# Performance work log

Hardware: AMD Instinct MI355X
Metric: run time of the kernel (lower is better)

## Reference

```python
import jax, jax.numpy as jnp
import numpy as np

B, G, D_EMB = 4096, 20000, 512
H_LOW, N_HIDDEN = 512, 1024
TOPK, T, FILM_W = 64, 0.1, 1.0
LN_EPS = 1e-5


def _layer_norm(x, gamma, beta):
    mu = jnp.mean(x, axis=-1, keepdims=True)
    var = jnp.mean(jnp.square(x - mu), axis=-1, keepdims=True)
    return (x - mu) * jax.lax.rsqrt(var + LN_EPS) * gamma + beta


def _l2norm(x, eps=1e-12):
    n = jnp.sqrt(jnp.sum(jnp.square(x), axis=-1, keepdims=True))
    return x / jnp.maximum(n, eps)


def setup_inputs() -> dict:
    key = jax.random.key(0)
    ks = jax.random.split(key, 8)
    s = 0.02
    return {
        "x": jax.random.normal(ks[0], (B, G), jnp.float32),
        "g": jax.random.normal(ks[1], (G, D_EMB), jnp.float32),
        "W_enc": jax.random.normal(ks[2], (H_LOW, G), jnp.float32) * s,
        "b_enc": jnp.zeros((H_LOW,), jnp.float32),
        "ln1_g": jnp.ones((H_LOW,), jnp.float32),
        "ln1_b": jnp.zeros((H_LOW,), jnp.float32),
        "W_ga": jax.random.normal(ks[3], (H_LOW, D_EMB), jnp.float32) * s,
        "W_gamma": jax.random.normal(ks[4], (H_LOW, H_LOW), jnp.float32) * s,
        "b_gamma": jnp.zeros((H_LOW,), jnp.float32),
        "W_beta": jax.random.normal(ks[5], (H_LOW, H_LOW), jnp.float32) * s,
        "b_beta": jnp.zeros((H_LOW,), jnp.float32),
        "W_exp": jax.random.normal(ks[6], (N_HIDDEN, H_LOW), jnp.float32) * s,
        "b_exp": jnp.zeros((N_HIDDEN,), jnp.float32),
        "ln2_g": jnp.ones((N_HIDDEN,), jnp.float32),
        "ln2_b": jnp.zeros((N_HIDDEN,), jnp.float32),
    }


def reference(x, g, W_enc, b_enc, ln1_g, ln1_b, W_ga, W_gamma, b_gamma,
              W_beta, b_beta, W_exp, b_exp, ln2_g, ln2_b):
    # x_encoder: Linear -> LayerNorm -> GELU (dropout = eval no-op)
    h = jnp.dot(x, W_enc.T) + b_enc                    # [B, H_LOW]
    h = jax.nn.gelu(_layer_norm(h, ln1_g, ln1_b), approximate=False)
    # gene adapter + cosine scores
    e = _l2norm(jnp.dot(g, W_ga.T))                    # [G, H_LOW]
    h_x = _l2norm(h)                                   # [B, H_LOW]
    scores = jnp.dot(h_x, e.T) / T                     # [B, G]
    # top-k mask + masked softmax attention
    _, idx = jax.lax.top_k(scores, TOPK)               # [B, TOPK]
    mask = jnp.zeros_like(scores).at[jnp.arange(B)[:, None], idx].set(1.0)
    attn = jax.nn.softmax(jnp.where(mask == 0, -1e9, scores), axis=-1)
    ctx = jnp.dot(attn, e)                             # [B, H_LOW]
    # FiLM (identity-centered)
    gamma = (jnp.dot(ctx, W_gamma.T) + b_gamma) * FILM_W
    beta = (jnp.dot(ctx, W_beta.T) + b_beta) * FILM_W
    h_cell = (1.0 + gamma) * h_x + beta
    # x_expand: Linear -> LayerNorm -> GELU
    h2 = jnp.dot(h_cell, W_exp.T) + b_exp              # [B, N_HIDDEN]
    return jax.nn.gelu(_layer_norm(h2, ln2_g, ln2_b), approximate=False)
```

## Files before the change

kernel.cpp:

```cpp
#include <hip/hip_runtime.h>
#include <hip/hip_fp16.h>
#include <math.h>
#include <type_traits>

#define DEVI __device__ __forceinline__

typedef __attribute__((ext_vector_type(8))) short bf16x8;
typedef __attribute__((ext_vector_type(4))) float f32x4;
typedef __attribute__((ext_vector_type(4))) unsigned int u32x4;
typedef unsigned short ushort_t;

DEVI unsigned int pack_bf16(float a, float b) {
  unsigned int ua = __float_as_uint(a), ub = __float_as_uint(b);
  ua = (ua + 0x7FFFu + ((ua >> 16) & 1u)) >> 16;
  ub = (ub + 0x7FFFu + ((ub >> 16) & 1u)) >> 16;
  return ua | (ub << 16);
}

DEVI bf16x8 cvt_bf16x8(f32x4 lo, f32x4 hi) {
  unsigned int r0, r1, r2, r3;
  asm("v_cvt_pk_bf16_f32 %0, %1, %2" : "=v"(r0) : "v"(lo[0]), "v"(lo[1]));
  asm("v_cvt_pk_bf16_f32 %0, %1, %2" : "=v"(r1) : "v"(lo[2]), "v"(lo[3]));
  asm("v_cvt_pk_bf16_f32 %0, %1, %2" : "=v"(r2) : "v"(hi[0]), "v"(hi[1]));
  asm("v_cvt_pk_bf16_f32 %0, %1, %2" : "=v"(r3) : "v"(hi[2]), "v"(hi[3]));
  union { u32x4 u; bf16x8 v; } x;
  x.u = u32x4{r0, r1, r2, r3};
  return x.v;
}

template<int SPLITZ, bool TAIL>
__global__ __launch_bounds__(512, 1) void bgemmA32(
    const float* __restrict__ A, const ushort_t* __restrict__ B,
    float* __restrict__ C, int M, int N, int K, int nbn, int nbm)
{
  __shared__ __align__(16) char L[131072];
  const int tid = threadIdx.x, lane = tid & 63, wv = tid >> 6;

  const int nwg = gridDim.x;
  const int hw = blockIdx.x;
  const int q = nwg >> 3, r = nwg & 7;
  const int xcd = hw & 7, pos = hw >> 3;
  const int lid = (xcd < r ? xcd * (q + 1) : r * (q + 1) + (xcd - r) * q) + pos;
  const int bn = lid % nbn;
  const int t2 = lid / nbn;
  const int bm = t2 % nbm;
  const int z  = t2 / nbm;

  const int ksteps = K >> 6;
  const int szk = (ksteps + SPLITZ - 1) / SPLITZ;
  const int kbBeg = z * szk;
  const int kbEnd = min(ksteps, kbBeg + szk);

  const int wm = wv >> 2, wn = wv & 3;
  const int lrow = lane & 15, kg = lane >> 4;

  f32x4 acc[4][4];
#pragma unroll
  for (int i = 0; i < 4; ++i)
#pragma unroll
    for (int j = 0; j < 4; ++j) acc[i][j] = f32x4{0.f, 0.f, 0.f, 0.f};

  const int alr = lane >> 3, ag32 = (lane & 7) >> 1;
  const float* aS[2];
#pragma unroll
  for (int j = 0; j < 2; ++j) {
    const int lr = (wv * 2 + j) * 8 + alr;
    const int swz = (lr ^ (lr >> 2)) & 3;
    const int colf = ((ag32 ^ swz) << 3) + (lane & 1) * 4;
    aS[j] = A + (size_t)min(bm * 128 + lr, M - 1) * (size_t)K + colf;
  }
  const int blr = lane >> 2, bgq = lane & 3;
  const ushort_t* bS[2];
#pragma unroll
  for (int j = 0; j < 2; ++j) {
    const int lr = (wv * 2 + j) * 16 + blr;
    const int swz = (lr ^ (lr >> 2)) & 3;
    aS[j] = aS[j];
    bS[j] = B + (size_t)min(bn * 256 + lr, N - 1) * (size_t)K + ((bgq ^ swz) << 3);
  }

  int offA[4], offB[4];
#pragma unroll
  for (int i = 0; i < 4; ++i) {
    const int ra = wm * 64 + i * 16 + lrow;
    offA[i] = ra * 128 + ((kg ^ ((ra ^ (ra >> 2)) & 3)) << 5);
  }
#pragma unroll
  for (int j = 0; j < 4; ++j) {
    const int rb = wn * 64 + j * 16 + lrow;
    offB[j] = rb * 64 + ((kg ^ ((rb ^ (rb >> 2)) & 3)) << 4);
  }

#define GA_STGA(h, k0v) do {                                                  \
    _Pragma("unroll")                                                         \
    for (int j_ = 0; j_ < 2; ++j_)                                            \
      __builtin_amdgcn_global_load_lds(                                       \
          (const __attribute__((address_space(1))) void*)(aS[j_] + (k0v) + (h) * 32), \
          (__attribute__((address_space(3))) void*)                           \
              (L + (s ^ 1) * 32768 + (h) * 16384 + (wv * 2 + j_) * 1024),     \
          16, 0, 0);                                                          \
  } while (0)
#define GA_STGB(h, k0v) do {                                                  \
    _Pragma("unroll")                                                         \
    for (int j_ = 0; j_ < 2; ++j_)                                            \
      __builtin_amdgcn_global_load_lds(                                       \
          (const __attribute__((address_space(1))) void*)(bS[j_] + (k0v) + (h) * 32), \
          (__attribute__((address_space(3))) void*)                           \
              (L + 65536 + (s ^ 1) * 32768 + (h) * 16384 + (wv * 2 + j_) * 1024), \
          16, 0, 0);                                                          \
  } while (0)
#define GA_RDB(h) do {                                                        \
    _Pragma("unroll")                                                         \
    for (int j_ = 0; j_ < 4; ++j_)                                            \
      bfv[j_] = *(const bf16x8*)(L + 65536 + s * 32768 + (h) * 16384 + offB[j_]); \
  } while (0)
#define GA_RDA(h, rg) do {                                                    \
    _Pragma("unroll")                                                         \
    for (int i_ = 0; i_ < 2; ++i_) {                                          \
      const char* pa_ = L + s * 32768 + (h) * 16384 + offA[(rg) * 2 + i_];    \
      af[i_] = cvt_bf16x8(*(const f32x4*)pa_, *(const f32x4*)(pa_ + 16));     \
    }                                                                         \
  } while (0)
#define GA_MM(rg) do {                                                        \
    _Pragma("unroll")                                                         \
    for (int i_ = 0; i_ < 2; ++i_)                                            \
      _Pragma("unroll")                                                       \
      for (int j_ = 0; j_ < 4; ++j_)                                          \
        acc[(rg) * 2 + i_][j_] = __builtin_amdgcn_mfma_f32_16x16x32_bf16(     \
            af[i_], bfv[j_], acc[(rg) * 2 + i_][j_], 0, 0, 0);                \
  } while (0)
#define GA_BAR asm volatile("s_barrier" ::: "memory")

  {
    int s = 1;
    const int k0 = kbBeg << 6;
    GA_STGA(0, k0); GA_STGB(0, k0); GA_STGA(1, k0); GA_STGB(1, k0);
  }
  asm volatile("s_waitcnt vmcnt(4)" ::: "memory");
  GA_BAR;

  int s = 0;
  for (int t = kbBeg; t < kbEnd; ++t) {
    const bool more = (t + 1 < kbEnd);
    const int k0n = (t + 1) << 6;
    bf16x8 af[2], bfv[4];
    GA_RDB(0); GA_RDA(0, 0);
    if (more) GA_STGA(0, k0n);
    GA_BAR;
    __builtin_amdgcn_s_setprio(1); GA_MM(0); __builtin_amdgcn_s_setprio(0);
    GA_BAR;
    GA_RDA(0, 1);
    if (more) GA_STGB(0, k0n);
    GA_BAR;
    __builtin_amdgcn_s_setprio(1); GA_MM(1); __builtin_amdgcn_s_setprio(0);
    if (more) asm volatile("s_waitcnt vmcnt(4)" ::: "memory");
    else      asm volatile("s_waitcnt vmcnt(0)" ::: "memory");
    GA_BAR;
    GA_RDB(1); GA_RDA(1, 0);
    if (more) GA_STGA(1, k0n);
    GA_BAR;
    __builtin_amdgcn_s_setprio(1); GA_MM(0); __builtin_amdgcn_s_setprio(0);
    GA_BAR;
    GA_RDA(1, 1);
    if (more) GA_STGB(1, k0n);
    GA_BAR;
    __builtin_amdgcn_s_setprio(1); GA_MM(1); __builtin_amdgcn_s_setprio(0);
    if (more) asm volatile("s_waitcnt vmcnt(4)" ::: "memory");
    GA_BAR;
    s ^= 1;
  }

  if (TAIL && z == SPLITZ - 1 && (K & 63)) {
    const int k0t = ksteps << 6;
    bf16x8 af[2], bfv[4];
#pragma unroll
    for (int j = 0; j < 2; ++j) {
      const float4 av = *(const float4*)(aS[j] + k0t);
      *(float4*)(L + s * 32768 + (wv * 2 + j) * 1024 + lane * 16) = av;
      const u32x4 bv = *(const u32x4*)(bS[j] + k0t);
      *(u32x4*)(L + 65536 + s * 32768 + (wv * 2 + j) * 1024 + lane * 16) = bv;
    }
    __syncthreads();
    GA_RDB(0);
    GA_RDA(0, 0); GA_MM(0);
    GA_RDA(0, 1); GA_MM(1);
  }
#undef GA_STGA
#undef GA_STGB
#undef GA_RDB
#undef GA_RDA
#undef GA_MM
#undef GA_BAR

  const size_t zoff = (SPLITZ > 1) ? (size_t)z * (size_t)M * (size_t)N : 0;
#pragma unroll
  for (int i = 0; i < 4; ++i) {
#pragma unroll
    for (int j = 0; j < 4; ++j) {
      const int col = bn * 256 + wn * 64 + j * 16 + lrow;
      if (col >= N) continue;
      const int row0 = bm * 128 + wm * 64 + i * 16 + kg * 4;
#pragma unroll
      for (int rr = 0; rr < 4; ++rr) {
        const int gr = row0 + rr;
        if (gr < M) C[zoff + (size_t)gr * (size_t)N + col] = acc[i][j][rr];
      }
    }
  }
}

template<int SPLITZ, typename OutT>
__global__ __launch_bounds__(512, 1) void bgemm256(
    const ushort_t* __restrict__ A, const ushort_t* __restrict__ B,
    OutT* __restrict__ C, int M, int N, int K, int nbn, int nbm)
{
  __shared__ __align__(16) char L[131072];
  const int tid = threadIdx.x, lane = tid & 63, wv = tid >> 6;

  const int nwg = gridDim.x;
  const int hw = blockIdx.x;
  const int q = nwg >> 3, r = nwg & 7;
  const int xcd = hw & 7, pos = hw >> 3;
  const int lid = (xcd < r ? xcd * (q + 1) : r * (q + 1) + (xcd - r) * q) + pos;
  const int bn = lid % nbn;
  const int t2 = lid / nbn;
  const int bm = t2 % nbm;
  const int z  = t2 / nbm;

  const int ksteps = K >> 6;
  int kbBeg = 0, kbEnd = ksteps;
  if (SPLITZ > 1) {
    const int sz = (ksteps + SPLITZ - 1) / SPLITZ;
    kbBeg = z * sz;
    kbEnd = min(ksteps, kbBeg + sz);
  }

  const int wm = wv >> 2, wn = wv & 3;
  const int lrow = lane & 15, kg = lane >> 4;

  f32x4 acc[8][4];
#pragma unroll
  for (int i = 0; i < 8; ++i)
#pragma unroll
    for (int j = 0; j < 4; ++j) acc[i][j] = f32x4{0.f, 0.f, 0.f, 0.f};

  const int sr = lane >> 2, sq = lane & 3;
  const ushort_t* aS[2];
  const ushort_t* bS[2];
#pragma unroll
  for (int j = 0; j < 2; ++j) {
    const int lr = (wv * 2 + j) * 16 + sr;
    const int swz = (lr ^ (lr >> 2)) & 3;
    aS[j] = A + (size_t)min(bm * 256 + lr, M - 1) * (size_t)K + ((sq ^ swz) << 3);
    bS[j] = B + (size_t)min(bn * 256 + lr, N - 1) * (size_t)K + ((sq ^ swz) << 3);
  }

  int offA[8], offB[4];
#pragma unroll
  for (int i = 0; i < 8; ++i) {
    const int ra = wm * 128 + i * 16 + lrow;
    offA[i] = ra * 64 + (((kg ^ ((ra ^ (ra >> 2)) & 3))) << 4);
  }
#pragma unroll
  for (int j = 0; j < 4; ++j) {
    const int rb = wn * 64 + j * 16 + lrow;
    offB[j] = rb * 64 + (((kg ^ ((rb ^ (rb >> 2)) & 3))) << 4);
  }

#define G256_STG(isB, h, k0v) do {                                            \
    _Pragma("unroll")                                                         \
    for (int j_ = 0; j_ < 2; ++j_)                                            \
      __builtin_amdgcn_global_load_lds(                                       \
          (const __attribute__((address_space(1))) void*)                     \
              (((isB) ? bS : aS)[j_] + (k0v) + (h) * 32),                     \
          (__attribute__((address_space(3))) void*)                           \
              (L + (isB) * 65536 + (s ^ 1) * 32768 + (h) * 16384 +            \
               (wv * 2 + j_) * 1024), 16, 0, 0);                              \
  } while (0)
#define G256_RDA(h, rg) do {                                                  \
    _Pragma("unroll")                                                         \
    for (int i_ = 0; i_ < 4; ++i_)                                            \
      af[i_] = *(const bf16x8*)(L + s * 32768 + (h) * 16384 +                 \
                                offA[(rg) * 4 + i_]);                         \
  } while (0)
#define G256_RDB(h) do {                                                      \
    _Pragma("unroll")                                                         \
    for (int j_ = 0; j_ < 4; ++j_)                                            \
      bfv[j_] = *(const bf16x8*)(L + 65536 + s * 32768 + (h) * 16384 +        \
                                 offB[j_]);                                   \
  } while (0)
#define G256_MM(rg) do {                                                      \
    _Pragma("unroll")                                                         \
    for (int i_ = 0; i_ < 4; ++i_)                                            \
      _Pragma("unroll")                                                       \
      for (int j_ = 0; j_ < 4; ++j_)                                          \
        acc[(rg) * 4 + i_][j_] = __builtin_amdgcn_mfma_f32_16x16x32_bf16(     \
            af[i_], bfv[j_], acc[(rg) * 4 + i_][j_], 0, 0, 0);                \
  } while (0)
#define G256_BAR asm volatile("s_barrier" ::: "memory")

  {
    int s = 1;
    const int k0 = kbBeg << 6;
    G256_STG(0, 0, k0);
    G256_STG(1, 0, k0);
    G256_STG(0, 1, k0);
    G256_STG(1, 1, k0);
  }
  asm volatile("s_waitcnt vmcnt(4)" ::: "memory");
  G256_BAR;

  int s = 0;
  for (int t = kbBeg; t < kbEnd; ++t) {
    const bool more = (t + 1 < kbEnd);
    const int k0n = (t + 1) << 6;
    bf16x8 af[4], bfv[4];
    G256_RDB(0);
    G256_RDA(0, 0);
    if (more) G256_STG(0, 0, k0n);
    G256_BAR;
    __builtin_amdgcn_s_setprio(1); G256_MM(0); __builtin_amdgcn_s_setprio(0);
    G256_BAR;
    G256_RDA(0, 1);
    if (more) G256_STG(1, 0, k0n);
    G256_BAR;
    __builtin_amdgcn_s_setprio(1); G256_MM(1); __builtin_amdgcn_s_setprio(0);
    if (more) asm volatile("s_waitcnt vmcnt(4)" ::: "memory");
    else      asm volatile("s_waitcnt vmcnt(0)" ::: "memory");
    G256_BAR;
    G256_RDB(1);
    G256_RDA(1, 0);
    if (more) G256_STG(0, 1, k0n);
    G256_BAR;
    __builtin_amdgcn_s_setprio(1); G256_MM(0); __builtin_amdgcn_s_setprio(0);
    G256_BAR;
    G256_RDA(1, 1);
    if (more) G256_STG(1, 1, k0n);
    G256_BAR;
    __builtin_amdgcn_s_setprio(1); G256_MM(1); __builtin_amdgcn_s_setprio(0);
    if (more) asm volatile("s_waitcnt vmcnt(4)" ::: "memory");
    G256_BAR;
    s ^= 1;
  }
#undef G256_STG
#undef G256_RDA
#undef G256_RDB
#undef G256_MM
#undef G256_BAR

  const size_t zoff = (SPLITZ > 1) ? (size_t)z * (size_t)M * (size_t)N : 0;
#pragma unroll
  for (int i = 0; i < 8; ++i) {
#pragma unroll
    for (int j = 0; j < 4; ++j) {
      const int col = bn * 256 + wn * 64 + j * 16 + lrow;
      if (col >= N) continue;
      const int row0 = bm * 256 + wm * 128 + i * 16 + kg * 4;
#pragma unroll
      for (int rr = 0; rr < 4; ++rr) {
        const int gr = row0 + rr;
        if (gr < M) {
          const float v = acc[i][j][rr];
          if constexpr (std::is_same<OutT, __half>::value)
            C[zoff + (size_t)gr * (size_t)N + col] = __float2half(v);
          else
            C[zoff + (size_t)gr * (size_t)N + col] = v;
        }
      }
    }
  }
}

template<typename AT, int SPLITZ, bool DUALB, bool BIAS, typename OutT>
__global__ __launch_bounds__(512, sizeof(AT) == 2 ? 3 : 2) void bgemm(
    const AT* __restrict__ A, const ushort_t* __restrict__ B0,
    const ushort_t* __restrict__ B1, const float* __restrict__ bias0,
    const float* __restrict__ bias1, OutT* __restrict__ C,
    int M, int N, int K, int nbn, int nbm)
{
  constexpr bool AB16 = (sizeof(AT) == 2);
  __shared__ __align__(16) char AsB[AB16 ? 16384 : 32768];
  __shared__ __align__(16) char BsB[32768];
  const int tid = threadIdx.x, lane = tid & 63, wv = tid >> 6;

  const int nwg = gridDim.x;
  const int hw = blockIdx.x;
  const int q = nwg >> 3, r = nwg & 7;
  const int xcd = hw & 7, pos = hw >> 3;
  const int lid = (xcd < r ? xcd * (q + 1) : r * (q + 1) + (xcd - r) * q) + pos;
  const int bn = lid % nbn;
  const int t2 = lid / nbn;
  const int bm = t2 % nbm;
  const int z  = t2 / nbm;

  const ushort_t* B  = (DUALB && z == 1) ? B1 : B0;
  const float* bias  = (DUALB && z == 1) ? bias1 : bias0;

  const int ksteps = (K + 63) >> 6;
  int kbBeg = 0, kbEnd = ksteps;
  if (SPLITZ > 1) {
    const int sz = (ksteps + SPLITZ - 1) / SPLITZ;
    kbBeg = z * sz;
    kbEnd = min(ksteps, kbBeg + sz);
  }

  const int wr = (wv >> 2) * 64;
  const int wc = (wv & 3) * 64;
  const int lrow = lane & 15, kg = lane >> 4;

  f32x4 acc[4][4];
#pragma unroll
  for (int i = 0; i < 4; ++i)
#pragma unroll
    for (int j = 0; j < 4; ++j) acc[i][j] = f32x4{0.f, 0.f, 0.f, 0.f};

  const AT* aSrc[4];
  if constexpr (AB16) {
    const int r0 = lane >> 3;
    const int ce = ((lane & 7) ^ r0) << 3;
#pragma unroll
    for (int j = 0; j < 2; ++j) {
      const int row = wv * 16 + j * 8 + r0;
      aSrc[j] = A + (size_t)min(bm * 128 + row, M - 1) * (size_t)K + ce;
    }
  } else {
    const int r0 = lane >> 4;
#pragma unroll
    for (int j = 0; j < 4; ++j) {
      const int row = wv * 16 + j * 4 + r0;
      const int ca = ((lane & 15) << 2) ^ ((row & 7) << 3);
      aSrc[j] = A + (size_t)min(bm * 128 + row, M - 1) * (size_t)K + ca;
    }
  }
  const int rB0 = lane >> 3;
  const int colB = ((lane & 7) ^ rB0) << 3;
  const ushort_t* bSrc[4];
#pragma unroll
  for (int j = 0; j < 4; ++j) {
    const int row = wv * 32 + j * 8 + rB0;
    bSrc[j] = B + (size_t)min(bn * 256 + row, N - 1) * (size_t)K + colB;
  }

  for (int kb = kbBeg; kb < kbEnd; ++kb) {
    const int k0 = kb << 6;
    if constexpr (AB16) {
#pragma unroll
      for (int j = 0; j < 2; ++j)
        __builtin_amdgcn_global_load_lds(
            (const __attribute__((address_space(1))) void*)(aSrc[j] + k0),
            (__attribute__((address_space(3))) void*)(AsB + (wv * 2 + j) * 1024),
            16, 0, 0);
    } else {
#pragma unroll
      for (int j = 0; j < 4; ++j)
        __builtin_amdgcn_global_load_lds(
            (const __attribute__((address_space(1))) void*)(aSrc[j] + k0),
            (__attribute__((address_space(3))) void*)(AsB + (wv * 4 + j) * 1024),
            16, 0, 0);
    }
#pragma unroll
    for (int j = 0; j < 4; ++j)
      __builtin_amdgcn_global_load_lds(
          (const __attribute__((address_space(1))) void*)(bSrc[j] + k0),
          (__attribute__((address_space(3))) void*)(BsB + (wv * 4 + j) * 1024),
          16, 0, 0);
    __syncthreads();
#pragma unroll
    for (int kk = 0; kk < 2; ++kk) {
      bf16x8 af[4], bfr[4];
#pragma unroll
      for (int i = 0; i < 4; ++i) {
        const int ra = wr + i * 16 + lrow;
        if constexpr (AB16) {
          af[i] = *(const bf16x8*)(AsB + ra * 128 + ((((kk << 2) + kg) ^ (ra & 7)) << 4));
        } else {
          const char* pa = AsB + ra * 256 + ((kk * 128 + (kg << 5)) ^ ((ra & 7) << 5));
          af[i] = cvt_bf16x8(*(const f32x4*)pa, *(const f32x4*)(pa + 16));
        }
        const int rb = wc + i * 16 + lrow;
        bfr[i] = *(const bf16x8*)(BsB + rb * 128 + ((((kk << 2) + kg) ^ (rb & 7)) << 4));
      }
#pragma unroll
      for (int i = 0; i < 4; ++i)
#pragma unroll
        for (int j = 0; j < 4; ++j)
          acc[i][j] = __builtin_amdgcn_mfma_f32_16x16x32_bf16(af[i], bfr[j], acc[i][j], 0, 0, 0);
    }
    __syncthreads();
  }

  const size_t zoff = (SPLITZ > 1 || DUALB) ? (size_t)z * (size_t)M * (size_t)N : 0;
#pragma unroll
  for (int i = 0; i < 4; ++i) {
#pragma unroll
    for (int j = 0; j < 4; ++j) {
      const int col = bn * 256 + wc + j * 16 + lrow;
      if (col >= N) continue;
      const int row0 = bm * 128 + wr + i * 16 + kg * 4;
      float bv = 0.f;
      if (BIAS) bv = bias[col];
#pragma unroll
      for (int rr = 0; rr < 4; ++rr) {
        const int gr = row0 + rr;
        if (gr < M) {
          const float v = acc[i][j][rr] + bv;
          if constexpr (std::is_same<OutT, __half>::value)
            C[zoff + (size_t)gr * (size_t)N + col] = __float2half(v);
          else
            C[zoff + (size_t)gr * (size_t)N + col] = v;
        }
      }
    }
  }
}

__global__ __launch_bounds__(256) void f2b(
    const float4* __restrict__ in, u32x4* __restrict__ out, int n8)
{
  const int i = blockIdx.x * 256 + threadIdx.x;
  if (i < n8) {
    const float4 a = in[2 * i], b = in[2 * i + 1];
    u32x4 o = { pack_bf16(a.x, a.y), pack_bf16(a.z, a.w),
                pack_bf16(b.x, b.y), pack_bf16(b.z, b.w) };
    out[i] = o;
  }
}

__global__ __launch_bounds__(256) void gee_fuse_ln1(
    const float* __restrict__ P, const float* __restrict__ b_enc,
    const float* __restrict__ g1, const float* __restrict__ b1,
    float* __restrict__ hx, unsigned int* __restrict__ hxb)
{
  const int row = blockIdx.x, tid = threadIdx.x;
  __shared__ float red[16];
  const size_t MN = (size_t)4096 * 512;
  const size_t o2 = (size_t)row * 256 + tid;
  float2 v = ((const float2*)b_enc)[tid];
#pragma unroll
  for (int qq = 0; qq < 4; ++qq) {
    const float2 p = ((const float2*)P)[qq * (MN / 2) + o2];
    v.x += p.x; v.y += p.y;
  }
  float a = v.x + v.y;
  float b = v.x * v.x + v.y * v.y;
#pragma unroll
  for (int o = 32; o > 0; o >>= 1) { a += __shfl_xor(a, o); b += __shfl_xor(b, o); }
  const int lane = tid & 63, wvi = tid >> 6;
  if (lane == 0) { red[wvi] = a; red[8 + wvi] = b; }
  __syncthreads();
  const float mu  = (red[0] + red[1] + red[2] + red[3]) * (1.f / 512.f);
  const float ex2 = (red[8] + red[9] + red[10] + red[11]) * (1.f / 512.f);
  const float inv = rsqrtf(ex2 - mu * mu + 1e-5f);
  const float2 gg = ((const float2*)g1)[tid];
  const float2 bb = ((const float2*)b1)[tid];
  const float y0 = (v.x - mu) * inv * gg.x + bb.x;
  const float y1 = (v.y - mu) * inv * gg.y + bb.y;
  const float t0 = 0.5f * y0 * (1.f + erff(y0 * 0.70710678118654752f));
  const float t1 = 0.5f * y1 * (1.f + erff(y1 * 0.70710678118654752f));
  float ss = t0 * t0 + t1 * t1;
  __syncthreads();
#pragma unroll
  for (int o = 32; o > 0; o >>= 1) ss += __shfl_xor(ss, o);
  if (lane == 0) red[wvi] = ss;
  __syncthreads();
  const float sc = 1.f / fmaxf(sqrtf(red[0] + red[1] + red[2] + red[3]), 1e-12f);
  const float h0 = t0 * sc, h1 = t1 * sc;
  ((float2*)hx)[o2] = make_float2(h0, h1);
  hxb[o2] = pack_bf16(h0, h1);
}

__global__ __launch_bounds__(256) void gee_l2rows(
    const __half2* __restrict__ ein, unsigned int* __restrict__ eb)
{
  const int row = blockIdx.x, tid = threadIdx.x;
  __shared__ float red[4];
  const __half2 h = ein[(size_t)row * 256 + tid];
  const float vx = __half2float(h.x), vy = __half2float(h.y);
  float ss = vx * vx + vy * vy;
#pragma unroll
  for (int o = 32; o > 0; o >>= 1) ss += __shfl_xor(ss, o);
  if ((tid & 63) == 0) red[tid >> 6] = ss;
  __syncthreads();
  const float sc = 1.f / fmaxf(sqrtf(red[0] + red[1] + red[2] + red[3]), 1e-12f);
  eb[(size_t)row * 256 + tid] = pack_bf16(vx * sc, vy * sc);
}

__global__ __launch_bounds__(256) void gee_topk_ctx(
    const __half* __restrict__ scores, const unsigned int* __restrict__ eb,
    unsigned int* __restrict__ ctxb)
{
  constexpr int G = 20000, GP = G / 2, CAP = 2048, TCAP = 160;
  const int row = blockIdx.x, tid = threadIdx.x;
  const int lane = tid & 63, wv = tid >> 6;
  __shared__ int hist[4][256];
  __shared__ int cnt_ge[256];
  __shared__ int wtop[4];
  __shared__ unsigned int comp[CAP];
  __shared__ int whist[4][16];
  __shared__ int sel[64];
  __shared__ float swt[64];
  __shared__ int tie[TCAP];
  __shared__ int s_thr, s_above, s_cand, s_cnt, s_n1, s_n2;

  const unsigned int* srow32 =
      (const unsigned int*)((const ushort_t*)scores + (size_t)row * G);
  const ushort_t* srow16 = (const ushort_t*)srow32;

#pragma unroll
  for (int b = 0; b < 4; ++b) hist[b][tid] = 0;
  if (tid == 0) { s_cnt = 0; s_n1 = 0; s_n2 = 0; }
  __syncthreads();

  for (int j0 = 0; j0 < GP; j0 += 256) {
    const int j = j0 + tid;
    if (j < GP) {
      const unsigned int p = srow32[j];
      const unsigned int f = (((p >> 15) & 0x10001u) * 0x7FFFu) + 0x80008000u;
      const unsigned int k2 = p ^ f;
      atomicAdd(&hist[wv][(k2 >> 8) & 0xFFu], 1);
      atomicAdd(&hist[wv][k2 >> 24], 1);
    }
  }
  __syncthreads();
  cnt_ge[tid] = hist[0][tid] + hist[1][tid] + hist[2][tid] + hist[3][tid];
  __syncthreads();
  for (int off = 1; off < 256; off <<= 1) {
    const int add = (tid + off < 256) ? cnt_ge[tid + off] : 0;
    __syncthreads();
    cnt_ge[tid] += add;
    __syncthreads();
  }
  {
    const unsigned long long m = __ballot(cnt_ge[tid] >= 64);
    if (lane == 0) wtop[wv] = m ? (wv * 64 + 63 - __clzll(m)) : -1;
  }
  __syncthreads();
  if (tid == 0) {
    const int thrB = max(max(wtop[0], wtop[1]), max(wtop[2], wtop[3]));
    s_cand  = cnt_ge[thrB];
    s_above = (thrB == 255) ? 0 : cnt_ge[thrB + 1];
    s_thr   = thrB << 8;
  }
  __syncthreads();

  const bool useComp = (s_cand <= CAP);
  const unsigned int thrB = ((unsigned int)s_thr) >> 8;

  if (useComp) {
    for (int j0 = 0; j0 < GP; j0 += 256) {
      const int j = j0 + tid;
      if (j < GP) {
        const unsigned int p = srow32[j];
        const unsigned int f = (((p >> 15) & 0x10001u) * 0x7FFFu) + 0x80008000u;
        const unsigned int k2 = p ^ f;
        const unsigned int lo = k2 & 0xFFFFu, hi = k2 >> 16;
        if ((lo >> 8) >= thrB) {
          const int pos = atomicAdd(&s_cnt, 1);
          comp[pos] = (lo << 16) | (unsigned)(2 * j);
        }
        if ((hi >> 8) >= thrB) {
          const int pos = atomicAdd(&s_cnt, 1);
          comp[pos] = (hi << 16) | (unsigned)(2 * j + 1);
        }
      }
    }
  }
  __syncthreads();
  const int Nloop = useComp ? s_cnt : G;

  for (int pass = 2; pass < 4; ++pass) {
    const int shift = 12 - 4 * pass;
    const unsigned int thr = (unsigned int)s_thr;
    const unsigned int pfx = thr >> (shift + 4);
    int c[16];
#pragma unroll
    for (int b = 0; b < 16; ++b) c[b] = 0;
    for (int j0 = 0; j0 < Nloop; j0 += 256) {
      const int j = j0 + tid;
      const bool ok = j < Nloop;
      unsigned int key;
      if (useComp) {
        key = ok ? (comp[j] >> 16) : 0u;
      } else {
        const unsigned int raw = ok ? (unsigned int)srow16[j] : 0u;
        key = (raw & 0x8000u) ? (0xFFFFu & ~raw) : (raw | 0x8000u);
      }
      const unsigned int nb = (ok && (key >> (shift + 4)) == pfx) ? ((key >> shift) & 15u) : 0xFFu;
#pragma unroll
      for (int b = 0; b < 16; ++b) c[b] += __popcll(__ballot(nb == (unsigned)b));
    }
    if (lane == 0) {
#pragma unroll
      for (int b = 0; b < 16; ++b) whist[wv][b] = c[b];
    }
    __syncthreads();
    if (tid == 0) {
      int run = s_above;
      for (int vv = 15; vv >= 0; --vv) {
        const int c4 = whist[0][vv] + whist[1][vv] + whist[2][vv] + whist[3][vv];
        if (run + c4 >= 64) { s_thr |= vv << shift; break; }
        run += c4;
      }
      s_above = run;
    }
    __syncthreads();
  }

  const unsigned int kthr = (unsigned int)s_thr;
  for (int j0 = 0; j0 < Nloop; j0 += 256) {
    const int j = j0 + tid;
    if (j < Nloop) {
      unsigned int key, idx;
      if (useComp) {
        const unsigned int u = comp[j];
        key = u >> 16; idx = u & 0xFFFFu;
      } else {
        const unsigned int raw = (unsigned int)srow16[j];
        key = (raw & 0x8000u) ? (0xFFFFu & ~raw) : (raw | 0x8000u);
        idx = (unsigned)j;
      }
      if (key > kthr) {
        const int pos = atomicAdd(&s_n1, 1);
        sel[pos] = (int)idx;
      } else if (key == kthr) {
        const int pos = atomicAdd(&s_n2, 1);
        if (pos < TCAP) tie[pos] = (int)idx;
      }
    }
  }
  __syncthreads();
  if (tid == 0) {
    const int n1 = s_n1;
    const int n2 = min(s_n2, TCAP);
    const int need = 64 - n1;
    for (int rr = 0; rr < need; ++rr) {
      int best = 1 << 30, bj = 0;
      for (int j = 0; j < n2; ++j)
        if (tie[j] < best) { best = tie[j]; bj = j; }
      sel[n1 + rr] = best;
      tie[bj] = 1 << 30;
    }
  }
  __syncthreads();
  if (tid < 64) {
    const int idx = sel[tid];
    const float sv = __half2float(scores[(size_t)row * G + idx]) * 10.0f;
    float m = sv;
#pragma unroll
    for (int o = 32; o > 0; o >>= 1) m = fmaxf(m, __shfl_xor(m, o));
    const float w = __expf(sv - m);
    float d = w;
#pragma unroll
    for (int o = 32; o > 0; o >>= 1) d += __shfl_xor(d, o);
    swt[tid] = w / d;
  }
  __syncthreads();
  float a0 = 0.f, a1 = 0.f;
#pragma unroll 4
  for (int k = 0; k < 64; ++k) {
    const unsigned int pk = eb[(size_t)sel[k] * 256 + tid];
    const float wk = swt[k];
    a0 += wk * __uint_as_float(pk << 16);
    a1 += wk * __uint_as_float(pk & 0xFFFF0000u);
  }
  ctxb[(size_t)row * 256 + tid] = pack_bf16(a0, a1);
}

__global__ __launch_bounds__(256) void gee_film(
    const float2* __restrict__ gm, const float2* __restrict__ bt,
    const float2* __restrict__ hx, unsigned int* __restrict__ hcb, int n2)
{
  const int i = blockIdx.x * 256 + threadIdx.x;
  if (i < n2) {
    const float2 g = gm[i], b = bt[i], h = hx[i];
    hcb[i] = pack_bf16((1.f + g.x) * h.x + b.x, (1.f + g.y) * h.y + b.y);
  }
}

__global__ __launch_bounds__(256) void gee_ln2(
    const float* __restrict__ h2, const float* __restrict__ g2,
    const float* __restrict__ b2, float* __restrict__ out)
{
  const int row = blockIdx.x, tid = threadIdx.x;
  __shared__ float red[16];
  float v[4];
  float a = 0.f, b = 0.f;
#pragma unroll
  for (int e = 0; e < 4; ++e) {
    v[e] = h2[(size_t)row * 1024 + tid + e * 256];
    a += v[e]; b += v[e] * v[e];
  }
#pragma unroll
  for (int o = 32; o > 0; o >>= 1) { a += __shfl_xor(a, o); b += __shfl_xor(b, o); }
  const int lane = tid & 63, wvi = tid >> 6;
  if (lane == 0) { red[wvi] = a; red[8 + wvi] = b; }
  __syncthreads();
  const float mu  = (red[0] + red[1] + red[2] + red[3]) * (1.f / 1024.f);
  const float ex2 = (red[8] + red[9] + red[10] + red[11]) * (1.f / 1024.f);
  const float inv = rsqrtf(ex2 - mu * mu + 1e-5f);
#pragma unroll
  for (int e = 0; e < 4; ++e) {
    const int c = tid + e * 256;
    const float y = (v[e] - mu) * inv * g2[c] + b2[c];
    out[(size_t)row * 1024 + c] = 0.5f * y * (1.f + erff(y * 0.70710678118654752f));
  }
}

extern "C" void kernel_launch(void* const* d_in, const int* in_sizes, int n_in,
                              void* d_out, int out_size, void* d_ws, size_t ws_size,
                              hipStream_t stream)
{
  const float* x       = (const float*)d_in[0];
  const float* g       = (const float*)d_in[1];
  const float* W_enc   = (const float*)d_in[2];
  const float* b_enc   = (const float*)d_in[3];
  const float* ln1_g   = (const float*)d_in[4];
  const float* ln1_b   = (const float*)d_in[5];
  const float* W_ga    = (const float*)d_in[6];
  const float* W_gamma = (const float*)d_in[7];
  const float* b_gamma = (const float*)d_in[8];
  const float* W_beta  = (const float*)d_in[9];
  const float* b_beta  = (const float*)d_in[10];
  const float* W_exp   = (const float*)d_in[11];
  const float* b_exp   = (const float*)d_in[12];
  const float* ln2_g   = (const float*)d_in[13];
  const float* ln2_b   = (const float*)d_in[14];
  float* out = (float*)d_out;

  char* ws = (char*)d_ws;
  constexpr size_t OFF_SCORES = 0;
  constexpr size_t OFF_GA     = 0;
  constexpr size_t OFF_BE     = 8388608;
  constexpr size_t OFF_H2     = 16777216;
  constexpr size_t OFF_PART   = 163840000;
  constexpr size_t OFF_WENCB  = 197394432;
  constexpr size_t OFF_E      = 197394432;
  constexpr size_t OFF_EB     = 217874432;
  constexpr size_t OFF_HX     = 238354432;
  constexpr size_t OFF_HXB    = 246743040;
  constexpr size_t OFF_CTXB   = 250937344;
  constexpr size_t OFF_HCB    = 255131648;
  constexpr size_t OFF_WGAB   = 259325952;
  constexpr size_t OFF_WGMB   = 259850240;
  constexpr size_t OFF_WBTB   = 260374528;
  constexpr size_t OFF_WEXB   = 260898816;

  __half*       scores = (__half*)(ws + OFF_SCORES);
  float*        ga     = (float*)(ws + OFF_GA);
  float*        be     = (float*)(ws + OFF_BE);
  float*        h2     = (float*)(ws + OFF_H2);
  float*        part   = (float*)(ws + OFF_PART);
  ushort_t*     wencb  = (ushort_t*)(ws + OFF_WENCB);
  __half*       e      = (__half*)(ws + OFF_E);
  unsigned int* eb     = (unsigned int*)(ws + OFF_EB);
  float*        hx     = (float*)(ws + OFF_HX);
  unsigned int* hxb    = (unsigned int*)(ws + OFF_HXB);
  unsigned int* ctxb   = (unsigned int*)(ws + OFF_CTXB);
  unsigned int* hcb    = (unsigned int*)(ws + OFF_HCB);
  ushort_t*     wgab   = (ushort_t*)(ws + OFF_WGAB);
  ushort_t*     wgmb   = (ushort_t*)(ws + OFF_WGMB);
  ushort_t*     wbtb   = (ushort_t*)(ws + OFF_WBTB);
  ushort_t*     wexb   = (ushort_t*)(ws + OFF_WEXB);

  f2b<<<5000, 256, 0, stream>>>((const float4*)W_enc,   (u32x4*)wencb, 1280000);
  f2b<<<128,  256, 0, stream>>>((const float4*)W_ga,    (u32x4*)wgab,  32768);
  f2b<<<128,  256, 0, stream>>>((const float4*)W_gamma, (u32x4*)wgmb,  32768);
  f2b<<<128,  256, 0, stream>>>((const float4*)W_beta,  (u32x4*)wbtb,  32768);
  f2b<<<256,  256, 0, stream>>>((const float4*)W_exp,   (u32x4*)wexb,  65536);

  bgemmA32<4, true><<<256, 512, 0, stream>>>(
      x, wencb, part, 4096, 512, 20000, 2, 32);
  gee_fuse_ln1<<<4096, 256, 0, stream>>>(part, b_enc, ln1_g, ln1_b, hx, hxb);
  bgemm<float, 1, false, false, __half><<<314, 512, 0, stream>>>(
      g, wgab, nullptr, nullptr, nullptr, e, 20000, 512, 512, 2, 157);
  gee_l2rows<<<20000, 256, 0, stream>>>((const __half2*)e, eb);
  bgemm256<1, __half><<<1264, 512, 0, stream>>>(
      (const ushort_t*)hxb, (const ushort_t*)eb, scores, 4096, 20000, 512, 79, 16);
  gee_topk_ctx<<<4096, 256, 0, stream>>>(scores, eb, ctxb);
  bgemm<ushort_t, 1, true, true, float><<<128, 512, 0, stream>>>(
      (const ushort_t*)ctxb, wgmb, wbtb, b_gamma, b_beta, ga, 4096, 512, 512, 2, 32);
  gee_film<<<4096, 256, 0, stream>>>((const float2*)ga, (const float2*)be,
                                     (const float2*)hx, hcb, 1048576);
  bgemm<ushort_t, 1, false, true, float><<<128, 512, 0, stream>>>(
      (const ushort_t*)hcb, wexb, nullptr, b_exp, nullptr, h2, 4096, 1024, 512, 4, 32);
  gee_ln2<<<4096, 256, 0, stream>>>(h2, ln2_g, ln2_b, out);
}
```

Baseline: 503.9 us.

## Fuse FiLM into dual gamma/beta GEMM and speculatively collect top-k candidates

A new bgemm_film kernel computes the gamma and beta projections together, sharing the A tile, and applies the FiLM combine in its epilogue, writing bf16 h_cell directly. This removes the separate gee_film kernel and the round trip of the fp32 gamma/beta buffers through memory. The top-k kernel now reads scores in 128-bit vectors and, during the histogram pass, speculatively gathers candidates whose high byte exceeds a fixed threshold (0xAD), so the second scan can be skipped when the real threshold lands above it. The fused GEMM uses only 64 workgroups and needs more LDS and registers, so occupancy and parallelism drop, and the speculative atomics add shared-memory contention.

```diff
diff --git a/kernel.cpp b/kernel.cpp
--- a/kernel.cpp
+++ b/kernel.cpp
@@ -15,6 +15,11 @@
   ua = (ua + 0x7FFFu + ((ua >> 16) & 1u)) >> 16;
   ub = (ub + 0x7FFFu + ((ub >> 16) & 1u)) >> 16;
   return ua | (ub << 16);
+}
+
+DEVI ushort_t rnd_bf16(float a) {
+  unsigned int ua = __float_as_uint(a);
+  return (ushort_t)((ua + 0x7FFFu + ((ua >> 16) & 1u)) >> 16);
 }
 
 DEVI bf16x8 cvt_bf16x8(f32x4 lo, f32x4 hi) {
@@ -75,7 +80,6 @@
   for (int j = 0; j < 2; ++j) {
     const int lr = (wv * 2 + j) * 16 + blr;
     const int swz = (lr ^ (lr >> 2)) & 3;
-    aS[j] = aS[j];
     bS[j] = B + (size_t)min(bn * 256 + lr, N - 1) * (size_t)K + ((bgq ^ swz) << 3);
   }
 
@@ -371,11 +375,10 @@
   }
 }
 
-template<typename AT, int SPLITZ, bool DUALB, bool BIAS, typename OutT>
+template<typename AT, int SPLITZ, bool BIAS, typename OutT>
 __global__ __launch_bounds__(512, sizeof(AT) == 2 ? 3 : 2) void bgemm(
     const AT* __restrict__ A, const ushort_t* __restrict__ B0,
-    const ushort_t* __restrict__ B1, const float* __restrict__ bias0,
-    const float* __restrict__ bias1, OutT* __restrict__ C,
+    const float* __restrict__ bias0, OutT* __restrict__ C,
     int M, int N, int K, int nbn, int nbm)
 {
   constexpr bool AB16 = (sizeof(AT) == 2);
@@ -393,8 +396,8 @@
   const int bm = t2 % nbm;
   const int z  = t2 / nbm;
 
-  const ushort_t* B  = (DUALB && z == 1) ? B1 : B0;
-  const float* bias  = (DUALB && z == 1) ? bias1 : bias0;
+  const ushort_t* B  = B0;
+  const float* bias  = bias0;
 
   const int ksteps = (K + 63) >> 6;
   int kbBeg = 0, kbEnd = ksteps;
@@ -489,7 +492,7 @@
     __syncthreads();
   }
 
-  const size_t zoff = (SPLITZ > 1 || DUALB) ? (size_t)z * (size_t)M * (size_t)N : 0;
+  const size_t zoff = (SPLITZ > 1) ? (size_t)z * (size_t)M * (size_t)N : 0;
 #pragma unroll
   for (int i = 0; i < 4; ++i) {
 #pragma unroll
@@ -509,6 +512,117 @@
           else
             C[zoff + (size_t)gr * (size_t)N + col] = v;
         }
+      }
+    }
+  }
+}
+
+__global__ __launch_bounds__(512, 2) void bgemm_film(
+    const ushort_t* __restrict__ A, const ushort_t* __restrict__ BG,
+    const ushort_t* __restrict__ BB, const float* __restrict__ bg,
+    const float* __restrict__ bb, const float* __restrict__ hx,
+    ushort_t* __restrict__ hcb)
+{
+  constexpr int M = 4096, N = 512, K = 512;
+  __shared__ __align__(16) char AsB[16384];
+  __shared__ __align__(16) char BsB[65536];
+  const int tid = threadIdx.x, lane = tid & 63, wv = tid >> 6;
+
+  const int nwg = gridDim.x;
+  const int hw = blockIdx.x;
+  const int q = nwg >> 3, r = nwg & 7;
+  const int xcd = hw & 7, pos = hw >> 3;
+  const int lid = (xcd < r ? xcd * (q + 1) : r * (q + 1) + (xcd - r) * q) + pos;
+  const int bn = lid % 2;
+  const int bm = lid / 2;
+
+  const int wr = (wv >> 2) * 64;
+  const int wc = (wv & 3) * 64;
+  const int lrow = lane & 15, kg = lane >> 4;
+
+  f32x4 accG[4][4], accB[4][4];
+#pragma unroll
+  for (int i = 0; i < 4; ++i)
+#pragma unroll
+    for (int j = 0; j < 4; ++j) {
+      accG[i][j] = f32x4{0.f, 0.f, 0.f, 0.f};
+      accB[i][j] = f32x4{0.f, 0.f, 0.f, 0.f};
+    }
+
+  const int r0 = lane >> 3;
+  const int ce = ((lane & 7) ^ r0) << 3;
+  const ushort_t* aSrc[2];
+#pragma unroll
+  for (int j = 0; j < 2; ++j) {
+    const int row = wv * 16 + j * 8 + r0;
+    aSrc[j] = A + (size_t)(bm * 128 + row) * (size_t)K + ce;
+  }
+  const ushort_t* gSrc[4];
+  const ushort_t* bSrc[4];
+#pragma unroll
+  for (int j = 0; j < 4; ++j) {
+    const int row = wv * 32 + j * 8 + r0;
+    gSrc[j] = BG + (size_t)(bn * 256 + row) * (size_t)K + ce;
+    bSrc[j] = BB + (size_t)(bn * 256 + row) * (size_t)K + ce;
+  }
+
+  for (int kb = 0; kb < K / 64; ++kb) {
+    const int k0 = kb << 6;
+#pragma unroll
+    for (int j = 0; j < 2; ++j)
+      __builtin_amdgcn_global_load_lds(
+          (const __attribute__((address_space(1))) void*)(aSrc[j] + k0),
+          (__attribute__((address_space(3))) void*)(AsB + (wv * 2 + j) * 1024),
+          16, 0, 0);
+#pragma unroll
+    for (int j = 0; j < 4; ++j) {
+      __builtin_amdgcn_global_load_lds(
+          (const __attribute__((address_space(1))) void*)(gSrc[j] + k0),
+          (__attribute__((address_space(3))) void*)(BsB + (wv * 4 + j) * 1024),
+          16, 0, 0);
+      __builtin_amdgcn_global_load_lds(
+          (const __attribute__((address_space(1))) void*)(bSrc[j] + k0),
+          (__attribute__((address_space(3))) void*)(BsB + 32768 + (wv * 4 + j) * 1024),
+          16, 0, 0);
+    }
+    __syncthreads();
+#pragma unroll
+    for (int kk = 0; kk < 2; ++kk) {
+      bf16x8 af[4], bfG[4], bfB[4];
+#pragma unroll
+      for (int i = 0; i < 4; ++i) {
+        const int ra = wr + i * 16 + lrow;
+        af[i] = *(const bf16x8*)(AsB + ra * 128 + ((((kk << 2) + kg) ^ (ra & 7)) << 4));
+        const int rb = wc + i * 16 + lrow;
+        const int bo = rb * 128 + ((((kk << 2) + kg) ^ (rb & 7)) << 4);
+        bfG[i] = *(const bf16x8*)(BsB + bo);
+        bfB[i] = *(const bf16x8*)(BsB + 32768 + bo);
+      }
+#pragma unroll
+      for (int i = 0; i < 4; ++i)
+#pragma unroll
+        for (int j = 0; j < 4; ++j) {
+          accG[i][j] = __builtin_amdgcn_mfma_f32_16x16x32_bf16(af[i], bfG[j], accG[i][j], 0, 0, 0);
+          accB[i][j] = __builtin_amdgcn_mfma_f32_16x16x32_bf16(af[i], bfB[j], accB[i][j], 0, 0, 0);
+        }
+    }
+    __syncthreads();
+  }
+
+#pragma unroll
+  for (int i = 0; i < 4; ++i) {
+#pragma unroll
+    for (int j = 0; j < 4; ++j) {
+      const int col = bn * 256 + wc + j * 16 + lrow;
+      const float gvb = bg[col], bvb = bb[col];
+      const int row0 = bm * 128 + wr + i * 16 + kg * 4;
+#pragma unroll
+      for (int rr = 0; rr < 4; ++rr) {
+        const int gr = row0 + rr;
+        const float gm = accG[i][j][rr] + gvb;
+        const float bt = accB[i][j][rr] + bvb;
+        const float h = hx[(size_t)gr * N + col];
+        hcb[(size_t)gr * N + col] = rnd_bf16((1.f + gm) * h + bt);
       }
     }
   }
@@ -589,7 +703,8 @@
     const __half* __restrict__ scores, const unsigned int* __restrict__ eb,
     unsigned int* __restrict__ ctxb)
 {
-  constexpr int G = 20000, GP = G / 2, CAP = 2048, TCAP = 160;
+  constexpr int G = 20000, GQ = G / 8, CAP = 2048, TCAP = 160;
+  constexpr unsigned int SPEC = 0xADu;
   const int row = blockIdx.x, tid = threadIdx.x;
   const int lane = tid & 63, wv = tid >> 6;
   __shared__ int hist[4][256];
@@ -602,23 +717,35 @@
   __shared__ int tie[TCAP];
   __shared__ int s_thr, s_above, s_cand, s_cnt, s_n1, s_n2;
 
-  const unsigned int* srow32 =
-      (const unsigned int*)((const ushort_t*)scores + (size_t)row * G);
-  const ushort_t* srow16 = (const ushort_t*)srow32;
+  const u32x4* srow128 = (const u32x4*)((const ushort_t*)scores + (size_t)row * G);
+  const ushort_t* srow16 = (const ushort_t*)srow128;
 
 #pragma unroll
   for (int b = 0; b < 4; ++b) hist[b][tid] = 0;
   if (tid == 0) { s_cnt = 0; s_n1 = 0; s_n2 = 0; }
   __syncthreads();
 
-  for (int j0 = 0; j0 < GP; j0 += 256) {
+  for (int j0 = 0; j0 < GQ; j0 += 256) {
     const int j = j0 + tid;
-    if (j < GP) {
-      const unsigned int p = srow32[j];
-      const unsigned int f = (((p >> 15) & 0x10001u) * 0x7FFFu) + 0x80008000u;
-      const unsigned int k2 = p ^ f;
-      atomicAdd(&hist[wv][(k2 >> 8) & 0xFFu], 1);
-      atomicAdd(&hist[wv][k2 >> 24], 1);
+    if (j < GQ) {
+      const u32x4 pv = srow128[j];
+#pragma unroll
+      for (int c = 0; c < 4; ++c) {
+        const unsigned int p = pv[c];
+        const unsigned int f = (((p >> 15) & 0x10001u) * 0x7FFFu) + 0x80008000u;
+        const unsigned int k2 = p ^ f;
+        const unsigned int bl = (k2 >> 8) & 0xFFu, bh = k2 >> 24;
+        atomicAdd(&hist[wv][bl], 1);
+        atomicAdd(&hist[wv][bh], 1);
+        if (bl >= SPEC) {
+          const int pp = atomicAdd(&s_cnt, 1);
+          if (pp < CAP) comp[pp] = ((k2 & 0xFFFFu) << 16) | (unsigned)(8 * j + 2 * c);
+        }
+        if (bh >= SPEC) {
+          const int pp = atomicAdd(&s_cnt, 1);
+          if (pp < CAP) comp[pp] = ((k2 >> 16) << 16) | (unsigned)(8 * j + 2 * c + 1);
+        }
+      }
     }
   }
   __syncthreads();
@@ -643,30 +770,39 @@
   }
   __syncthreads();
 
-  const bool useComp = (s_cand <= CAP);
   const unsigned int thrB = ((unsigned int)s_thr) >> 8;
-
-  if (useComp) {
-    for (int j0 = 0; j0 < GP; j0 += 256) {
+  const int specCnt = cnt_ge[SPEC];
+  const bool useSpec = (thrB >= SPEC) && (specCnt <= CAP);
+  const bool useComp = useSpec || (s_cand <= CAP);
+
+  if (!useSpec && useComp) {
+    __syncthreads();
+    if (tid == 0) s_cnt = 0;
+    __syncthreads();
+    for (int j0 = 0; j0 < GQ; j0 += 256) {
       const int j = j0 + tid;
-      if (j < GP) {
-        const unsigned int p = srow32[j];
-        const unsigned int f = (((p >> 15) & 0x10001u) * 0x7FFFu) + 0x80008000u;
-        const unsigned int k2 = p ^ f;
-        const unsigned int lo = k2 & 0xFFFFu, hi = k2 >> 16;
-        if ((lo >> 8) >= thrB) {
-          const int pos = atomicAdd(&s_cnt, 1);
-          comp[pos] = (lo << 16) | (unsigned)(2 * j);
+      if (j < GQ) {
+        const u32x4 pv = srow128[j];
+#pragma unroll
+        for (int c = 0; c < 4; ++c) {
+          const unsigned int p = pv[c];
+          const unsigned int f = (((p >> 15) & 0x10001u) * 0x7FFFu) + 0x80008000u;
+          const unsigned int k2 = p ^ f;
+          const unsigned int lo = k2 & 0xFFFFu, hi = k2 >> 16;
+          if ((lo >> 8) >= thrB) {
+            const int pp = atomicAdd(&s_cnt, 1);
+            comp[pp] = (lo << 16) | (unsigned)(8 * j + 2 * c);
+          }
+          if ((hi >> 8) >= thrB) {
+            const int pp = atomicAdd(&s_cnt, 1);
+            comp[pp] = (hi << 16) | (unsigned)(8 * j + 2 * c + 1);
+          }
         }
-        if ((hi >> 8) >= thrB) {
-          const int pos = atomicAdd(&s_cnt, 1);
-          comp[pos] = (hi << 16) | (unsigned)(2 * j + 1);
-        }
-      }
-    }
-  }
-  __syncthreads();
-  const int Nloop = useComp ? s_cnt : G;
+      }
+    }
+  }
+  __syncthreads();
+  const int Nloop = useComp ? min(s_cnt, CAP) : G;
 
   for (int pass = 2; pass < 4; ++pass) {
     const int shift = 12 - 4 * pass;
@@ -720,11 +856,11 @@
         idx = (unsigned)j;
       }
       if (key > kthr) {
-        const int pos = atomicAdd(&s_n1, 1);
-        sel[pos] = (int)idx;
+        const int pp = atomicAdd(&s_n1, 1);
+        sel[pp] = (int)idx;
       } else if (key == kthr) {
-        const int pos = atomicAdd(&s_n2, 1);
-        if (pos < TCAP) tie[pos] = (int)idx;
+        const int pp = atomicAdd(&s_n2, 1);
+        if (pp < TCAP) tie[pp] = (int)idx;
       }
     }
   }
@@ -764,17 +900,6 @@
     a1 += wk * __uint_as_float(pk & 0xFFFF0000u);
   }
   ctxb[(size_t)row * 256 + tid] = pack_bf16(a0, a1);
-}
-
-__global__ __launch_bounds__(256) void gee_film(
-    const float2* __restrict__ gm, const float2* __restrict__ bt,
-    const float2* __restrict__ hx, unsigned int* __restrict__ hcb, int n2)
-{
-  const int i = blockIdx.x * 256 + threadIdx.x;
-  if (i < n2) {
-    const float2 g = gm[i], b = bt[i], h = hx[i];
-    hcb[i] = pack_bf16((1.f + g.x) * h.x + b.x, (1.f + g.y) * h.y + b.y);
-  }
 }
 
 __global__ __launch_bounds__(256) void gee_ln2(
@@ -829,9 +954,7 @@
 
   char* ws = (char*)d_ws;
   constexpr size_t OFF_SCORES = 0;
-  constexpr size_t OFF_GA     = 0;
-  constexpr size_t OFF_BE     = 8388608;
-  constexpr size_t OFF_H2     = 16777216;
+  constexpr size_t OFF_H2     = 0;
   constexpr size_t OFF_PART   = 163840000;
   constexpr size_t OFF_WENCB  = 197394432;
   constexpr size_t OFF_E      = 197394432;
@@ -846,8 +969,6 @@
   constexpr size_t OFF_WEXB   = 260898816;
 
   __half*       scores = (__half*)(ws + OFF_SCORES);
-  float*        ga     = (float*)(ws + OFF_GA);
-  float*        be     = (float*)(ws + OFF_BE);
   float*        h2     = (float*)(ws + OFF_H2);
   float*        part   = (float*)(ws + OFF_PART);
   ushort_t*     wencb  = (ushort_t*)(ws + OFF_WENCB);
@@ -856,7 +977,7 @@
   float*        hx     = (float*)(ws + OFF_HX);
   unsigned int* hxb    = (unsigned int*)(ws + OFF_HXB);
   unsigned int* ctxb   = (unsigned int*)(ws + OFF_CTXB);
-  unsigned int* hcb    = (unsigned int*)(ws + OFF_HCB);
+  ushort_t*     hcb    = (ushort_t*)(ws + OFF_HCB);
   ushort_t*     wgab   = (ushort_t*)(ws + OFF_WGAB);
   ushort_t*     wgmb   = (ushort_t*)(ws + OFF_WGMB);
   ushort_t*     wbtb   = (ushort_t*)(ws + OFF_WBTB);
@@ -871,17 +992,15 @@
   bgemmA32<4, true><<<256, 512, 0, stream>>>(
       x, wencb, part, 4096, 512, 20000, 2, 32);
   gee_fuse_ln1<<<4096, 256, 0, stream>>>(part, b_enc, ln1_g, ln1_b, hx, hxb);
-  bgemm<float, 1, false, false, __half><<<314, 512, 0, stream>>>(
-      g, wgab, nullptr, nullptr, nullptr, e, 20000, 512, 512, 2, 157);
+  bgemm<float, 1, false, __half><<<314, 512, 0, stream>>>(
+      g, wgab, nullptr, e, 20000, 512, 512, 2, 157);
   gee_l2rows<<<20000, 256, 0, stream>>>((const __half2*)e, eb);
   bgemm256<1, __half><<<1264, 512, 0, stream>>>(
       (const ushort_t*)hxb, (const ushort_t*)eb, scores, 4096, 20000, 512, 79, 16);
   gee_topk_ctx<<<4096, 256, 0, stream>>>(scores, eb, ctxb);
-  bgemm<ushort_t, 1, true, true, float><<<128, 512, 0, stream>>>(
-      (const ushort_t*)ctxb, wgmb, wbtb, b_gamma, b_beta, ga, 4096, 512, 512, 2, 32);
-  gee_film<<<4096, 256, 0, stream>>>((const float2*)ga, (const float2*)be,
-                                     (const float2*)hx, hcb, 1048576);
-  bgemm<ushort_t, 1, false, true, float><<<128, 512, 0, stream>>>(
-      (const ushort_t*)hcb, wexb, nullptr, b_exp, nullptr, h2, 4096, 1024, 512, 4, 32);
+  bgemm_film<<<64, 512, 0, stream>>>(
+      (const ushort_t*)ctxb, wgmb, wbtb, b_gamma, b_beta, hx, hcb);
+  bgemm<ushort_t, 1, true, float><<<128, 512, 0, stream>>>(
+      hcb, wexb, b_exp, h2, 4096, 1024, 512, 4, 32);
   gee_ln2<<<4096, 256, 0, stream>>>(h2, ln2_g, ln2_b, out);
 }
```

New measurement: 481.5 us. 4.4% less time.
